# Kernel tuning notes

Measured on AMD Instinct MI355X. Metric: run time of the kernel, lower is better.

## Reference

```python
import jax, jax.numpy as jnp
import numpy as np

B, S, D, H, HD = 1, 4096, 1024, 16, 64
HALF = HD // 2


def setup_inputs() -> dict:
    key = jax.random.key(0)
    ks = jax.random.split(key, 8)
    std = 0.02
    x = jax.random.normal(ks[0], (B, S, D), dtype=jnp.float32)
    wq_w = jax.random.normal(ks[1], (D, D), dtype=jnp.float32) * std
    wk_w = jax.random.normal(ks[2], (D, D), dtype=jnp.float32) * std
    wv_w = jax.random.normal(ks[3], (D, D), dtype=jnp.float32) * std
    wo_w = jax.random.normal(ks[4], (D, D), dtype=jnp.float32) * std
    wq_b = jnp.zeros((D,), jnp.float32)
    wk_b = jnp.zeros((D,), jnp.float32)
    wv_b = jnp.zeros((D,), jnp.float32)
    wo_b = jnp.zeros((D,), jnp.float32)
    # LLaMA-style rotary frequencies: theta = 10000^{-2i/HD}
    inv_freq = 1.0 / (10000.0 ** (jnp.arange(0, HD, 2, dtype=jnp.float32) / HD))  # [HALF]
    t = jnp.arange(S, dtype=jnp.float32)
    angles = jnp.outer(t, inv_freq)  # [S, HALF]
    freqs_cos = jnp.cos(angles)
    freqs_sin = jnp.sin(angles)
    # causal additive mask (finite large-negative to stay grad-safe)
    mask = jnp.triu(jnp.full((S, S), -1e9, dtype=jnp.float32), k=1)[None, None]
    return {
        "x": x, "start_pos": 0, "freqs_cos": freqs_cos, "freqs_sin": freqs_sin,
        "mask": mask,
        "wq_w": wq_w, "wq_b": wq_b, "wk_w": wk_w, "wk_b": wk_b,
        "wv_w": wv_w, "wv_b": wv_b, "wo_w": wo_w, "wo_b": wo_b,
    }


def _apply_rope(t, cos, sin):
    # t: [B, S, H, HD]; cos/sin: [S, HALF]. Complex multiply on consecutive pairs.
    b, s, h, hd = t.shape
    t2 = t.reshape(b, s, h, hd // 2, 2)
    x0, x1 = t2[..., 0], t2[..., 1]
    c = cos[None, :, None, :]
    sn = sin[None, :, None, :]
    o0 = x0 * c - x1 * sn
    o1 = x0 * sn + x1 * c
    return jnp.stack([o0, o1], axis=-1).reshape(b, s, h, hd)


def reference(x, start_pos, freqs_cos, freqs_sin, mask,
              wq_w, wq_b, wk_w, wk_b, wv_w, wv_b, wo_w, wo_b):
    bsz, seqlen, dim = x.shape
    q = (x @ wq_w.T + wq_b).reshape(bsz, seqlen, H, HD)
    k = (x @ wk_w.T + wk_b).reshape(bsz, seqlen, H, HD)
    v = (x @ wv_w.T + wv_b).reshape(bsz, seqlen, H, HD)
    q = _apply_rope(q, freqs_cos, freqs_sin)
    k = _apply_rope(k, freqs_cos, freqs_sin)
    # [B, H, S, HD]
    q = q.transpose(0, 2, 1, 3)
    k = k.transpose(0, 2, 1, 3)
    v = v.transpose(0, 2, 1, 3)
    scores = jnp.einsum('bhqd,bhkd->bhqk', q, k) / jnp.sqrt(jnp.float32(HD))
    scores = scores + mask
    probs = jax.nn.softmax(scores.astype(jnp.float32), axis=-1).astype(q.dtype)
    out = jnp.einsum('bhqk,bhkd->bhqd', probs, v)  # [B, H, S, HD]
    out = out.transpose(0, 2, 1, 3).reshape(bsz, seqlen, dim)
    return out @ wo_w.T + wo_b
```

## Files before the change

### kernel.cpp

```cpp
#include <hip/hip_runtime.h>


#define S_LEN 4096
#define DIM   1024
#define NH    16
#define HD    64

typedef __attribute__((ext_vector_type(8))) short bf16x8;
typedef __attribute__((ext_vector_type(4))) float f32x4;

__device__ __forceinline__ unsigned short f2b(float f) {
  union { float f; unsigned int u; } v; v.f = f;
  unsigned int r = (v.u + 0x7fffu + ((v.u >> 16) & 1u)) >> 16;
  return (unsigned short)r;
}
__device__ __forceinline__ float b2f(unsigned short h) {
  union { unsigned int u; float f; } v; v.u = ((unsigned int)h) << 16;
  return v.f;
}
__device__ __forceinline__ unsigned int pk2t(float a, float b) {
  union { float f; unsigned int u; } x, y; x.f = a; y.f = b;
  return (x.u >> 16) | (y.u & 0xffff0000u);
}
__device__ __forceinline__ void gload16(const void* g, void* l) {
  __builtin_amdgcn_global_load_lds(
      (const __attribute__((address_space(1))) unsigned int*)g,
      (__attribute__((address_space(3))) unsigned int*)l, 16, 0, 0);
}
__device__ __forceinline__ f32x4 fzero4() { f32x4 z = {0.f, 0.f, 0.f, 0.f}; return z; }

__global__ void cvt_all(const float* __restrict__ x, const float* __restrict__ wq,
                        const float* __restrict__ wk, const float* __restrict__ wv,
                        const float* __restrict__ wo, const float* __restrict__ qb,
                        const float* __restrict__ kb, const float* __restrict__ vbs,
                        const float* __restrict__ ob, unsigned short* __restrict__ xb,
                        unsigned short* __restrict__ wqkvb, unsigned short* __restrict__ wobb,
                        float* __restrict__ biasq, float* __restrict__ biaso) {
  int i = blockIdx.x * 256 + threadIdx.x;
  if (i < 2097152) {
    const float* src; unsigned short* dst; int off;
    if (i < 1048576)      { src = x;  dst = xb;              off = i; }
    else if (i < 1310720) { src = wq; dst = wqkvb;           off = i - 1048576; }
    else if (i < 1572864) { src = wk; dst = wqkvb + 1048576; off = i - 1310720; }
    else if (i < 1835008) { src = wv; dst = wqkvb + 2097152; off = i - 1572864; }
    else                  { src = wo; dst = wobb;            off = i - 1835008; }
    float4 v = ((const float4*)src)[off];
    unsigned int lo = (unsigned int)f2b(v.x) | ((unsigned int)f2b(v.y) << 16);
    unsigned int hi = (unsigned int)f2b(v.z) | ((unsigned int)f2b(v.w) << 16);
    ((uint2*)dst)[off] = make_uint2(lo, hi);
  } else if (i < 2097152 + 1024) {
    int j = i - 2097152;
    if (j < 256)      ((float4*)biasq)[j]              = ((const float4*)qb)[j];
    else if (j < 512) ((float4*)(biasq + 1024))[j-256] = ((const float4*)kb)[j-256];
    else if (j < 768) ((float4*)(biasq + 2048))[j-512] = ((const float4*)vbs)[j-512];
    else              ((float4*)biaso)[j-768]          = ((const float4*)ob)[j-768];
  }
}

__global__ __launch_bounds__(256) void gemm_qkv(
    const unsigned short* __restrict__ A, const unsigned short* __restrict__ B,
    const float* __restrict__ bias, unsigned short* __restrict__ dq,
    unsigned short* __restrict__ dk, unsigned short* __restrict__ vtout,
    const float* __restrict__ fc, const float* __restrict__ fs, int K) {
  __shared__ alignas(16) unsigned short sA[2][128 * 32];
  __shared__ alignas(16) unsigned short sB[2][128 * 32];
  const int tid = threadIdx.x;
  const int lane = tid & 63, wave = tid >> 6;
  const int ln = lane & 15, quad = lane >> 4;
  const int bm = blockIdx.x * 128, bn = blockIdx.y * 128;
  const int wr = (wave >> 1) * 64, wc = (wave & 1) * 64;

  f32x4 acc[4][4];
#pragma unroll
  for (int i = 0; i < 4; ++i)
#pragma unroll
    for (int j = 0; j < 4; ++j) acc[i][j] = fzero4();

#pragma unroll
  for (int i = 0; i < 2; ++i) {
    int o = (i * 256 + tid) * 16;
    int e = o >> 1;
    int row = e >> 5, col = e & 31;
    gload16(A + (size_t)(bm + row) * K + col, (char*)sA[0] + o);
    gload16(B + (size_t)(bn + row) * K + col, (char*)sB[0] + o);
  }

  int buf = 0;
  for (int k0 = 0; k0 < K; k0 += 32, buf ^= 1) {
    __syncthreads();
    if (k0 + 32 < K) {
#pragma unroll
      for (int i = 0; i < 2; ++i) {
        int o = (i * 256 + tid) * 16;
        int e = o >> 1;
        int row = e >> 5, col = e & 31;
        gload16(A + (size_t)(bm + row) * K + k0 + 32 + col, (char*)sA[buf ^ 1] + o);
        gload16(B + (size_t)(bn + row) * K + k0 + 32 + col, (char*)sB[buf ^ 1] + o);
      }
    }
    bf16x8 af[4], bfr[4];
#pragma unroll
    for (int i = 0; i < 4; ++i) {
      af[i]  = *(const bf16x8*)&sA[buf][(wr + i * 16 + ln) * 32 + quad * 8];
      bfr[i] = *(const bf16x8*)&sB[buf][(wc + i * 16 + ln) * 32 + quad * 8];
    }
#pragma unroll
    for (int i = 0; i < 4; ++i)
#pragma unroll
      for (int j = 0; j < 4; ++j)
        acc[i][j] = __builtin_amdgcn_mfma_f32_16x16x32_bf16(af[i], bfr[j], acc[i][j], 0, 0, 0);
  }

  const int bufi = bn >> 10;
  const int hq = ((bn & 1023) + wc) >> 6;
  if (bufi < 2) {
    unsigned short* const base = bufi == 0 ? dq : dk;
    const float qsc = bufi == 0 ? 0.180336880f : 1.0f;
#pragma unroll
    for (int i = 0; i < 4; ++i)
#pragma unroll
      for (int j = 0; j < 4; ++j) {
        int n = bn + wc + j * 16 + ln;
        float bi = bias[n];
        int hd = j * 16 + ln;
        int pi = hd >> 1;
        bool evn = (ln & 1) == 0;
#pragma unroll
        for (int r = 0; r < 4; ++r) {
          int m = bm + wr + i * 16 + quad * 4 + r;
          float val = acc[i][j][r] + bi;
          float par = __shfl_xor(val, 1);
          float c = fc[m * 32 + pi], sn = fs[m * 32 + pi];
          float o = evn ? (val * c - par * sn) : (par * sn + val * c);
          base[((size_t)(hq * S_LEN + m)) * HD + hd] = f2b(o * qsc);
        }
      }
  } else {
    __syncthreads();
    unsigned short* scr =
        (wave < 2 ? (unsigned short*)sA : (unsigned short*)sB) + (wave & 1) * 4096;
#pragma unroll
    for (int i = 0; i < 4; ++i)
#pragma unroll
      for (int j = 0; j < 4; ++j) {
        int n = bn + wc + j * 16 + ln;
        float bi = bias[n];
        int hd = j * 16 + ln;
#pragma unroll
        for (int r = 0; r < 4; ++r) {
          int sl = i * 16 + quad * 4 + r;
          int byte = hd * 128 + ((((sl >> 3) ^ (hd & 7)) << 4)) + (sl & 7) * 2;
          *(unsigned short*)((char*)scr + byte) = f2b(acc[i][j][r] + bi);
        }
      }
#pragma unroll
    for (int pass = 0; pass < 4; ++pass) {
      int row = pass * 16 + ln;
      uint4 d0 = *(uint4*)((char*)scr + row * 128 + (((quad * 2) ^ (row & 7)) << 4));
      uint4 d1 = *(uint4*)((char*)scr + row * 128 + (((quad * 2 + 1) ^ (row & 7)) << 4));
      uint4* dst = (uint4*)(vtout + ((size_t)(hq * HD + row)) * S_LEN + bm + wr + quad * 16);
      dst[0] = d0;
      dst[1] = d1;
    }
  }
}

__global__ __launch_bounds__(256) void gemm_out(
    const unsigned short* __restrict__ A, const unsigned short* __restrict__ B,
    const float* __restrict__ bias, float* __restrict__ outF, int N, int K) {
  __shared__ alignas(16) unsigned short sA[2][128 * 32];
  __shared__ alignas(16) unsigned short sB[2][64 * 32];
  const int tid = threadIdx.x;
  const int lane = tid & 63, wave = tid >> 6;
  const int ln = lane & 15, quad = lane >> 4;
  const int bm = blockIdx.x * 128, bn = blockIdx.y * 64;
  const int wr = (wave >> 1) * 64, wc = (wave & 1) * 32;

  f32x4 acc[4][2];
#pragma unroll
  for (int i = 0; i < 4; ++i)
#pragma unroll
    for (int j = 0; j < 2; ++j) acc[i][j] = fzero4();

  {
#pragma unroll
    for (int i = 0; i < 2; ++i) {
      int o = (i * 256 + tid) * 16;
      int e = o >> 1;
      int row = e >> 5, col = e & 31;
      gload16(A + (size_t)(bm + row) * K + col, (char*)sA[0] + o);
    }
    int o = tid * 16;
    int e = o >> 1;
    int row = e >> 5, col = e & 31;
    gload16(B + (size_t)(bn + row) * K + col, (char*)sB[0] + o);
  }

  int buf = 0;
  for (int k0 = 0; k0 < K; k0 += 32, buf ^= 1) {
    __syncthreads();
    if (k0 + 32 < K) {
#pragma unroll
      for (int i = 0; i < 2; ++i) {
        int o = (i * 256 + tid) * 16;
        int e = o >> 1;
        int row = e >> 5, col = e & 31;
        gload16(A + (size_t)(bm + row) * K + k0 + 32 + col, (char*)sA[buf ^ 1] + o);
      }
      int o = tid * 16;
      int e = o >> 1;
      int row = e >> 5, col = e & 31;
      gload16(B + (size_t)(bn + row) * K + k0 + 32 + col, (char*)sB[buf ^ 1] + o);
    }
    bf16x8 af[4], bfr[2];
#pragma unroll
    for (int i = 0; i < 4; ++i)
      af[i] = *(const bf16x8*)&sA[buf][(wr + i * 16 + ln) * 32 + quad * 8];
#pragma unroll
    for (int j = 0; j < 2; ++j)
      bfr[j] = *(const bf16x8*)&sB[buf][(wc + j * 16 + ln) * 32 + quad * 8];
#pragma unroll
    for (int i = 0; i < 4; ++i)
#pragma unroll
      for (int j = 0; j < 2; ++j)
        acc[i][j] = __builtin_amdgcn_mfma_f32_16x16x32_bf16(af[i], bfr[j], acc[i][j], 0, 0, 0);
  }

#pragma unroll
  for (int i = 0; i < 4; ++i)
#pragma unroll
    for (int j = 0; j < 2; ++j) {
      int n = bn + wc + j * 16 + ln;
      float bi = bias[n];
#pragma unroll
      for (int r = 0; r < 4; ++r) {
        int m = bm + wr + i * 16 + quad * 4 + r;
        outF[(size_t)m * N + n] = acc[i][j][r] + bi;
      }
    }
}

__device__ __forceinline__ bf16x8 lds_swzK(const unsigned short* s, int row, int chunk) {
  int byte = row * 128 + ((chunk ^ ((row >> 2) & 7)) << 4);
  return *(const bf16x8*)((const char*)s + byte);
}
__device__ __forceinline__ bf16x8 lds_swzV(const unsigned short* s, int row, int chunk) {
  int byte = row * 128 + ((chunk ^ (row & 7)) << 4);
  return *(const bf16x8*)((const char*)s + byte);
}

__global__ __launch_bounds__(512, 2) void flash_kernel(
    const unsigned short* __restrict__ qg, const unsigned short* __restrict__ kg,
    const unsigned short* __restrict__ vtg, unsigned short* __restrict__ attn) {
  __shared__ alignas(16) unsigned short sK[2][64 * 64];
  __shared__ alignas(16) unsigned short sV[2][64 * 64];
  __shared__ alignas(16) unsigned short sP[8 * 16 * 72];

  const int tid = threadIdx.x;
  const int lane = tid & 63, wave = tid >> 6;
  const int w = wave & 3, grp = wave >> 2;
  const int ln = lane & 15, quad = lane >> 4;
  const int c = blockIdx.x;
  const int h = 2 * (c & 7) + ((c >> 3) & 1);
  const int u = c >> 4;
  const int a = (u < 16) ? u : 47 - u;
  const int q0 = (grp == 0 ? a : 63 - a) * 64;
  const int qrow = q0 + w * 16;

  const unsigned short* qh = qg + (size_t)h * (S_LEN * HD);
  const unsigned short* kh = kg + (size_t)h * (S_LEN * HD);
  const unsigned short* vh = vtg + (size_t)h * (HD * S_LEN);

  bf16x8 qf[2];
  qf[0] = *(const bf16x8*)(qh + (size_t)(qrow + ln) * HD + quad * 8);
  qf[1] = *(const bf16x8*)(qh + (size_t)(qrow + ln) * HD + 32 + quad * 8);

  f32x4 o_acc[4];
  f32x4 l_acc = fzero4();
#pragma unroll
  for (int t = 0; t < 4; ++t) o_acc[t] = fzero4();
  bf16x8 ones;
#pragma unroll
  for (int j = 0; j < 8; ++j) ones[j] = (short)0x3F80;
  unsigned short* pw = &sP[wave * (16 * 72)];

  const int nkv = 64 - a;
  const int srow = tid >> 3, sch = tid & 7;

  gload16(kh + (size_t)srow * HD + ((sch ^ ((srow >> 2) & 7)) << 3), (char*)sK[0] + tid * 16);
  gload16(vh + (size_t)srow * S_LEN + ((sch ^ (srow & 7)) << 3), (char*)sV[0] + tid * 16);

  int buf = 0;
  for (int kt = 0; kt < nkv; ++kt, buf ^= 1) {
    const int kv0 = kt * 64;
    __syncthreads();
    if (kt + 1 < nkv) {
      const int kv1 = kv0 + 64;
      gload16(kh + (size_t)(kv1 + srow) * HD + ((sch ^ ((srow >> 2) & 7)) << 3),
              (char*)sK[buf ^ 1] + tid * 16);
      gload16(vh + (size_t)srow * S_LEN + kv1 + ((sch ^ (srow & 7)) << 3),
              (char*)sV[buf ^ 1] + tid * 16);
    }
    if (kv0 > qrow + 15) continue;

    const unsigned short* kp = sK[buf];
    const unsigned short* vp = sV[buf];
    f32x4 sc[4];
#pragma unroll
    for (int t = 0; t < 4; ++t) sc[t] = fzero4();
#pragma unroll
    for (int t = 0; t < 4; ++t) {
      int krow = ln * 4 + t;
      bf16x8 kb0 = lds_swzK(kp, krow, quad);
      bf16x8 kb1 = lds_swzK(kp, krow, 4 + quad);
      sc[t] = __builtin_amdgcn_mfma_f32_16x16x32_bf16(qf[0], kb0, sc[t], 0, 0, 0);
      sc[t] = __builtin_amdgcn_mfma_f32_16x16x32_bf16(qf[1], kb1, sc[t], 0, 0, 0);
    }

    if (kv0 == q0) {
#pragma unroll
      for (int r = 0; r < 4; ++r) {
        int row = qrow + quad * 4 + r;
        int colb = kv0 + ln * 4;
        float p0 = (colb + 0 <= row) ? __builtin_amdgcn_exp2f(sc[0][r]) : 0.0f;
        float p1 = (colb + 1 <= row) ? __builtin_amdgcn_exp2f(sc[1][r]) : 0.0f;
        float p2 = (colb + 2 <= row) ? __builtin_amdgcn_exp2f(sc[2][r]) : 0.0f;
        float p3 = (colb + 3 <= row) ? __builtin_amdgcn_exp2f(sc[3][r]) : 0.0f;
        *(uint2*)&pw[(quad * 4 + r) * 72 + ln * 4] = make_uint2(pk2t(p0, p1), pk2t(p2, p3));
      }
    } else {
#pragma unroll
      for (int r = 0; r < 4; ++r) {
        float p0 = __builtin_amdgcn_exp2f(sc[0][r]);
        float p1 = __builtin_amdgcn_exp2f(sc[1][r]);
        float p2 = __builtin_amdgcn_exp2f(sc[2][r]);
        float p3 = __builtin_amdgcn_exp2f(sc[3][r]);
        *(uint2*)&pw[(quad * 4 + r) * 72 + ln * 4] = make_uint2(pk2t(p0, p1), pk2t(p2, p3));
      }
    }

    bf16x8 pa0 = *(const bf16x8*)&pw[ln * 72 + quad * 8];
    bf16x8 pa1 = *(const bf16x8*)&pw[ln * 72 + 32 + quad * 8];

    l_acc = __builtin_amdgcn_mfma_f32_16x16x32_bf16(pa0, ones, l_acc, 0, 0, 0);
    l_acc = __builtin_amdgcn_mfma_f32_16x16x32_bf16(pa1, ones, l_acc, 0, 0, 0);

#pragma unroll
    for (int t = 0; t < 4; ++t) {
      int vrow = t * 16 + ln;
      bf16x8 vb0 = lds_swzV(vp, vrow, quad);
      bf16x8 vb1 = lds_swzV(vp, vrow, 4 + quad);
      o_acc[t] = __builtin_amdgcn_mfma_f32_16x16x32_bf16(pa0, vb0, o_acc[t], 0, 0, 0);
      o_acc[t] = __builtin_amdgcn_mfma_f32_16x16x32_bf16(pa1, vb1, o_acc[t], 0, 0, 0);
    }
  }

  float inv[4];
#pragma unroll
  for (int r = 0; r < 4; ++r) inv[r] = 1.0f / l_acc[r];
#pragma unroll
  for (int t = 0; t < 4; ++t)
#pragma unroll
    for (int r = 0; r < 4; ++r) {
      int row = qrow + quad * 4 + r;
      attn[(size_t)row * DIM + h * HD + t * 16 + ln] = f2b(o_acc[t][r] * inv[r]);
    }
}

extern "C" void kernel_launch(void* const* d_in, const int* in_sizes, int n_in,
                              void* d_out, int out_size, void* d_ws, size_t ws_size,
                              hipStream_t stream) {
  const float* x    = (const float*)d_in[0];
  const float* fc   = (const float*)d_in[2];
  const float* fs   = (const float*)d_in[3];
  const float* wqw  = (const float*)d_in[5];
  const float* wqb  = (const float*)d_in[6];
  const float* wkw  = (const float*)d_in[7];
  const float* wkb  = (const float*)d_in[8];
  const float* wvw  = (const float*)d_in[9];
  const float* wvb  = (const float*)d_in[10];
  const float* wow  = (const float*)d_in[11];
  const float* wobf = (const float*)d_in[12];
  float* out = (float*)d_out;

  char* ws = (char*)d_ws;
  const size_t MB = (size_t)1 << 20;
  unsigned short* xb    = (unsigned short*)(ws + 0);
  unsigned short* wqkvb = (unsigned short*)(ws + 8 * MB);
  unsigned short* wobb  = (unsigned short*)(ws + 16 * MB);
  float* biasq = (float*)(ws + 18 * MB);
  float* biaso = (float*)(ws + 18 * MB + 65536);
  unsigned short* qb_ = (unsigned short*)(ws + 19 * MB);
  unsigned short* kb_ = (unsigned short*)(ws + 27 * MB);
  unsigned short* vt  = (unsigned short*)(ws + 35 * MB);
  unsigned short* attn = (unsigned short*)(ws + 0);

  cvt_all<<<8196, 256, 0, stream>>>(x, wqw, wkw, wvw, wow, wqb, wkb, wvb, wobf,
                                    xb, wqkvb, wobb, biasq, biaso);
  gemm_qkv<<<dim3(32, 24), 256, 0, stream>>>(xb, wqkvb, biasq, qb_, kb_, vt, fc, fs, 1024);
  flash_kernel<<<512, 512, 0, stream>>>(qb_, kb_, vt, attn);
  gemm_out<<<dim3(32, 16), 256, 0, stream>>>(attn, wobb, biaso, out, 1024, 1024);
}
```

Measured before the change: 266.5 us.

## Split KV range across wave groups, compute S transposed, use permlane instead of LDS

New measurement: 249.8 us. 6.3% less time.

```diff
diff --git a/kernel.cpp b/kernel.cpp
--- a/kernel.cpp
+++ b/kernel.cpp
@@ -240,32 +240,25 @@
     }
 }
 
-__device__ __forceinline__ bf16x8 lds_swzK(const unsigned short* s, int row, int chunk) {
-  int byte = row * 128 + ((chunk ^ ((row >> 2) & 7)) << 4);
-  return *(const bf16x8*)((const char*)s + byte);
-}
-__device__ __forceinline__ bf16x8 lds_swzV(const unsigned short* s, int row, int chunk) {
+__device__ __forceinline__ bf16x8 lds_swz(const unsigned short* s, int row, int chunk) {
   int byte = row * 128 + ((chunk ^ (row & 7)) << 4);
   return *(const bf16x8*)((const char*)s + byte);
 }
 
-__global__ __launch_bounds__(512, 2) void flash_kernel(
+__global__ __launch_bounds__(512, 4) void flash_kernel(
     const unsigned short* __restrict__ qg, const unsigned short* __restrict__ kg,
     const unsigned short* __restrict__ vtg, unsigned short* __restrict__ attn) {
-  __shared__ alignas(16) unsigned short sK[2][64 * 64];
-  __shared__ alignas(16) unsigned short sV[2][64 * 64];
-  __shared__ alignas(16) unsigned short sP[8 * 16 * 72];
+  __shared__ alignas(16) unsigned short sK[2][2][64 * 64];
+  __shared__ alignas(16) unsigned short sV[2][2][64 * 64];
 
   const int tid = threadIdx.x;
   const int lane = tid & 63, wave = tid >> 6;
   const int w = wave & 3, grp = wave >> 2;
   const int ln = lane & 15, quad = lane >> 4;
   const int c = blockIdx.x;
-  const int h = 2 * (c & 7) + ((c >> 3) & 1);
-  const int u = c >> 4;
-  const int a = (u < 16) ? u : 47 - u;
-  const int q0 = (grp == 0 ? a : 63 - a) * 64;
-  const int qrow = q0 + w * 16;
+  const int h = c & 15;
+  const int qt = 63 - (c >> 4);
+  const int qrow = qt * 64 + w * 16;
 
   const unsigned short* qh = qg + (size_t)h * (S_LEN * HD);
   const unsigned short* kh = kg + (size_t)h * (S_LEN * HD);
@@ -282,89 +275,116 @@
   bf16x8 ones;
 #pragma unroll
   for (int j = 0; j < 8; ++j) ones[j] = (short)0x3F80;
-  unsigned short* pw = &sP[wave * (16 * 72)];
-
-  const int nkv = 64 - a;
+
+  const int nst = (qt + 2) >> 1;
   const int srow = tid >> 3, sch = tid & 7;
-
-  gload16(kh + (size_t)srow * HD + ((sch ^ ((srow >> 2) & 7)) << 3), (char*)sK[0] + tid * 16);
-  gload16(vh + (size_t)srow * S_LEN + ((sch ^ (srow & 7)) << 3), (char*)sV[0] + tid * 16);
+  const int kswz = (sch ^ (srow & 7)) << 3;
+
+  gload16(kh + (size_t)srow * HD + kswz, (char*)sK[0][0] + tid * 16);
+  gload16(kh + (size_t)(64 + srow) * HD + kswz, (char*)sK[0][1] + tid * 16);
+  gload16(vh + (size_t)srow * S_LEN + kswz, (char*)sV[0][0] + tid * 16);
+  gload16(vh + (size_t)srow * S_LEN + 64 + kswz, (char*)sV[0][1] + tid * 16);
 
   int buf = 0;
-  for (int kt = 0; kt < nkv; ++kt, buf ^= 1) {
+  for (int s = 0; s < nst; ++s, buf ^= 1) {
+    __syncthreads();
+    if (s + 1 < nst) {
+      const int kvE = (2 * s + 2) * 64, kvO = kvE + 64;
+      gload16(kh + (size_t)(kvE + srow) * HD + kswz, (char*)sK[buf ^ 1][0] + tid * 16);
+      gload16(kh + (size_t)(kvO + srow) * HD + kswz, (char*)sK[buf ^ 1][1] + tid * 16);
+      gload16(vh + (size_t)srow * S_LEN + kvE + kswz, (char*)sV[buf ^ 1][0] + tid * 16);
+      gload16(vh + (size_t)srow * S_LEN + kvO + kswz, (char*)sV[buf ^ 1][1] + tid * 16);
+    }
+    const int kt = 2 * s + grp;
+    if (kt > qt) continue;
     const int kv0 = kt * 64;
-    __syncthreads();
-    if (kt + 1 < nkv) {
-      const int kv1 = kv0 + 64;
-      gload16(kh + (size_t)(kv1 + srow) * HD + ((sch ^ ((srow >> 2) & 7)) << 3),
-              (char*)sK[buf ^ 1] + tid * 16);
-      gload16(vh + (size_t)srow * S_LEN + kv1 + ((sch ^ (srow & 7)) << 3),
-              (char*)sV[buf ^ 1] + tid * 16);
-    }
-    if (kv0 > qrow + 15) continue;
-
-    const unsigned short* kp = sK[buf];
-    const unsigned short* vp = sV[buf];
+    const unsigned short* kp = sK[buf][grp];
+    const unsigned short* vp = sV[buf][grp];
+
     f32x4 sc[4];
 #pragma unroll
     for (int t = 0; t < 4; ++t) sc[t] = fzero4();
 #pragma unroll
     for (int t = 0; t < 4; ++t) {
-      int krow = ln * 4 + t;
-      bf16x8 kb0 = lds_swzK(kp, krow, quad);
-      bf16x8 kb1 = lds_swzK(kp, krow, 4 + quad);
-      sc[t] = __builtin_amdgcn_mfma_f32_16x16x32_bf16(qf[0], kb0, sc[t], 0, 0, 0);
-      sc[t] = __builtin_amdgcn_mfma_f32_16x16x32_bf16(qf[1], kb1, sc[t], 0, 0, 0);
-    }
-
-    if (kv0 == q0) {
+      bf16x8 kb0 = lds_swz(kp, t * 16 + ln, quad);
+      bf16x8 kb1 = lds_swz(kp, t * 16 + ln, 4 + quad);
+      sc[t] = __builtin_amdgcn_mfma_f32_16x16x32_bf16(kb0, qf[0], sc[t], 0, 0, 0);
+      sc[t] = __builtin_amdgcn_mfma_f32_16x16x32_bf16(kb1, qf[1], sc[t], 0, 0, 0);
+    }
+
+    float e[4][4];
+    if (kt == qt) {
+#pragma unroll
+      for (int t = 0; t < 4; ++t)
+#pragma unroll
+        for (int r = 0; r < 4; ++r) {
+          int kvl = 16 * t + quad * 4 + r;
+          e[t][r] = (kvl <= w * 16 + ln) ? __builtin_amdgcn_exp2f(sc[t][r]) : 0.0f;
+        }
+    } else {
+#pragma unroll
+      for (int t = 0; t < 4; ++t)
+#pragma unroll
+        for (int r = 0; r < 4; ++r) e[t][r] = __builtin_amdgcn_exp2f(sc[t][r]);
+    }
+
+    unsigned int x0 = pk2t(e[0][0], e[0][1]), x1 = pk2t(e[0][2], e[0][3]);
+    unsigned int y0 = pk2t(e[1][0], e[1][1]), y1 = pk2t(e[1][2], e[1][3]);
+    unsigned int z0 = pk2t(e[2][0], e[2][1]), z1 = pk2t(e[2][2], e[2][3]);
+    unsigned int w0 = pk2t(e[3][0], e[3][1]), w1 = pk2t(e[3][2], e[3][3]);
+    auto a32 = __builtin_amdgcn_permlane32_swap(x0, y0, false, false);
+    auto a16 = __builtin_amdgcn_permlane16_swap(a32[0], a32[1], false, false);
+    auto b32 = __builtin_amdgcn_permlane32_swap(x1, y1, false, false);
+    auto b16 = __builtin_amdgcn_permlane16_swap(b32[0], b32[1], false, false);
+    auto c32 = __builtin_amdgcn_permlane32_swap(z0, w0, false, false);
+    auto c16 = __builtin_amdgcn_permlane16_swap(c32[0], c32[1], false, false);
+    auto d32 = __builtin_amdgcn_permlane32_swap(z1, w1, false, false);
+    auto d16 = __builtin_amdgcn_permlane16_swap(d32[0], d32[1], false, false);
+    union { uint4 u; bf16x8 b; } pa0u, pa1u;
+    pa0u.u = make_uint4(a16[0], b16[0], a16[1], b16[1]);
+    pa1u.u = make_uint4(c16[0], d16[0], c16[1], d16[1]);
+    const bf16x8 pa0 = pa0u.b, pa1 = pa1u.b;
+
+    l_acc = __builtin_amdgcn_mfma_f32_16x16x32_bf16(pa0, ones, l_acc, 0, 0, 0);
+    l_acc = __builtin_amdgcn_mfma_f32_16x16x32_bf16(pa1, ones, l_acc, 0, 0, 0);
+
+#pragma unroll
+    for (int t = 0; t < 4; ++t) {
+      bf16x8 vb0 = lds_swz(vp, t * 16 + ln, quad);
+      bf16x8 vb1 = lds_swz(vp, t * 16 + ln, 4 + quad);
+      o_acc[t] = __builtin_amdgcn_mfma_f32_16x16x32_bf16(pa0, vb0, o_acc[t], 0, 0, 0);
+      o_acc[t] = __builtin_amdgcn_mfma_f32_16x16x32_bf16(pa1, vb1, o_acc[t], 0, 0, 0);
+    }
+  }
+
+  __syncthreads();
+  float* mrg = (float*)sK;
+  const int mi = (w * 64 + lane) * 20;
+  if (grp == 1) {
+    *(f32x4*)&mrg[mi +  0] = o_acc[0];
+    *(f32x4*)&mrg[mi +  4] = o_acc[1];
+    *(f32x4*)&mrg[mi +  8] = o_acc[2];
+    *(f32x4*)&mrg[mi + 12] = o_acc[3];
+    *(f32x4*)&mrg[mi + 16] = l_acc;
+  }
+  __syncthreads();
+  if (grp == 0) {
+    o_acc[0] += *(const f32x4*)&mrg[mi + 0];
+    o_acc[1] += *(const f32x4*)&mrg[mi + 4];
+    o_acc[2] += *(const f32x4*)&mrg[mi + 8];
+    o_acc[3] += *(const f32x4*)&mrg[mi + 12];
+    l_acc += *(const f32x4*)&mrg[mi + 16];
+    float inv[4];
+#pragma unroll
+    for (int r = 0; r < 4; ++r) inv[r] = 1.0f / l_acc[r];
+#pragma unroll
+    for (int t = 0; t < 4; ++t)
 #pragma unroll
       for (int r = 0; r < 4; ++r) {
         int row = qrow + quad * 4 + r;
-        int colb = kv0 + ln * 4;
-        float p0 = (colb + 0 <= row) ? __builtin_amdgcn_exp2f(sc[0][r]) : 0.0f;
-        float p1 = (colb + 1 <= row) ? __builtin_amdgcn_exp2f(sc[1][r]) : 0.0f;
-        float p2 = (colb + 2 <= row) ? __builtin_amdgcn_exp2f(sc[2][r]) : 0.0f;
-        float p3 = (colb + 3 <= row) ? __builtin_amdgcn_exp2f(sc[3][r]) : 0.0f;
-        *(uint2*)&pw[(quad * 4 + r) * 72 + ln * 4] = make_uint2(pk2t(p0, p1), pk2t(p2, p3));
-      }
-    } else {
-#pragma unroll
-      for (int r = 0; r < 4; ++r) {
-        float p0 = __builtin_amdgcn_exp2f(sc[0][r]);
-        float p1 = __builtin_amdgcn_exp2f(sc[1][r]);
-        float p2 = __builtin_amdgcn_exp2f(sc[2][r]);
-        float p3 = __builtin_amdgcn_exp2f(sc[3][r]);
-        *(uint2*)&pw[(quad * 4 + r) * 72 + ln * 4] = make_uint2(pk2t(p0, p1), pk2t(p2, p3));
-      }
-    }
-
-    bf16x8 pa0 = *(const bf16x8*)&pw[ln * 72 + quad * 8];
-    bf16x8 pa1 = *(const bf16x8*)&pw[ln * 72 + 32 + quad * 8];
-
-    l_acc = __builtin_amdgcn_mfma_f32_16x16x32_bf16(pa0, ones, l_acc, 0, 0, 0);
-    l_acc = __builtin_amdgcn_mfma_f32_16x16x32_bf16(pa1, ones, l_acc, 0, 0, 0);
-
-#pragma unroll
-    for (int t = 0; t < 4; ++t) {
-      int vrow = t * 16 + ln;
-      bf16x8 vb0 = lds_swzV(vp, vrow, quad);
-      bf16x8 vb1 = lds_swzV(vp, vrow, 4 + quad);
-      o_acc[t] = __builtin_amdgcn_mfma_f32_16x16x32_bf16(pa0, vb0, o_acc[t], 0, 0, 0);
-      o_acc[t] = __builtin_amdgcn_mfma_f32_16x16x32_bf16(pa1, vb1, o_acc[t], 0, 0, 0);
-    }
-  }
-
-  float inv[4];
-#pragma unroll
-  for (int r = 0; r < 4; ++r) inv[r] = 1.0f / l_acc[r];
-#pragma unroll
-  for (int t = 0; t < 4; ++t)
-#pragma unroll
-    for (int r = 0; r < 4; ++r) {
-      int row = qrow + quad * 4 + r;
-      attn[(size_t)row * DIM + h * HD + t * 16 + ln] = f2b(o_acc[t][r] * inv[r]);
-    }
+        attn[(size_t)row * DIM + h * HD + t * 16 + ln] = f2b(o_acc[t][r] * inv[r]);
+      }
+  }
 }
 
 extern "C" void kernel_launch(void* const* d_in, const int* in_sizes, int n_in,
@@ -398,6 +418,6 @@
   cvt_all<<<8196, 256, 0, stream>>>(x, wqw, wkw, wvw, wow, wqb, wkb, wvb, wobf,
                                     xb, wqkvb, wobb, biasq, biaso);
   gemm_qkv<<<dim3(32, 24), 256, 0, stream>>>(xb, wqkvb, biasq, qb_, kb_, vt, fc, fs, 1024);
-  flash_kernel<<<512, 512, 0, stream>>>(qb_, kb_, vt, attn);
+  flash_kernel<<<1024, 512, 0, stream>>>(qb_, kb_, vt, attn);
   gemm_out<<<dim3(32, 16), 256, 0, stream>>>(attn, wobb, biaso, out, 1024, 1024);
 }
```
